# Performance work log

Measured on AMD Instinct MI355X. Metric: run time of the kernel, lower is better.

## Reference

```python
import jax, jax.numpy as jnp
import numpy as np

DIM = 2048
NUM_HEADS = 16
HEAD_DIM = DIM // NUM_HEADS  # 128
LATENT = 512
THETA = 10000.0


def rotate_half(x):
    # interleaved rotate: (x0,x1,x2,x3,...) -> (-x1,x0,-x3,x2,...)
    x1 = x[..., ::2]
    x2 = x[..., 1::2]
    return jnp.stack((-x2, x1), axis=-1).reshape(x.shape)


def apply_rope(x, sin, cos):
    return x * cos + rotate_half(x) * sin


def setup_inputs() -> dict:
    key = jax.random.key(0)
    ks = jax.random.split(key, 6)
    s_in = 1.0 / np.sqrt(DIM)
    s_lat = 1.0 / np.sqrt(LATENT)
    x = jax.random.normal(ks[0], (2, 2048, DIM), dtype=jnp.float32)
    Wq = jax.random.normal(ks[1], (DIM, DIM), dtype=jnp.float32) * s_in
    Wdkv = jax.random.normal(ks[2], (DIM, 2 * LATENT), dtype=jnp.float32) * s_in
    Wuk = jax.random.normal(ks[3], (LATENT, DIM), dtype=jnp.float32) * s_lat
    Wuv = jax.random.normal(ks[4], (LATENT, DIM), dtype=jnp.float32) * s_lat
    Wo = jax.random.normal(ks[5], (DIM, DIM), dtype=jnp.float32) * s_in
    return {"x": x, "Wq": Wq, "Wdkv": Wdkv, "Wuk": Wuk, "Wuv": Wuv, "Wo": Wo}


def reference(x, Wq, Wdkv, Wuk, Wuv, Wo):
    b, s, _ = x.shape
    # q projection -> [b, h, s, hd]
    q = (x @ Wq).reshape(b, s, NUM_HEADS, HEAD_DIM).transpose(0, 2, 1, 3)
    # low-rank latent down-projection, then up-project K and V
    dkv = x @ Wdkv  # [b, s, 2*L]
    dk, dv = dkv[..., :LATENT], dkv[..., LATENT:]
    k = (dk @ Wuk).reshape(b, s, NUM_HEADS, HEAD_DIM).transpose(0, 2, 1, 3)
    v = (dv @ Wuv).reshape(b, s, NUM_HEADS, HEAD_DIM).transpose(0, 2, 1, 3)
    # RoPE cache (concatenated freqs, matching the torch module)
    inv_freq = 1.0 / (THETA ** (jnp.arange(0, HEAD_DIM, 2, dtype=jnp.float32) / HEAD_DIM))
    t = jnp.arange(s, dtype=jnp.float32)
    freqs = t[:, None] * inv_freq[None, :]          # [s, hd/2]
    emb = jnp.concatenate([freqs, freqs], axis=-1)  # [s, hd]
    sin, cos = jnp.sin(emb), jnp.cos(emb)
    q = apply_rope(q, sin, cos)
    k = apply_rope(k, sin, cos)
    # SDPA (no mask, no dropout): scale = 1/sqrt(head_dim)
    scores = jnp.einsum('bhqd,bhkd->bhqk', q, k) / jnp.sqrt(jnp.float32(HEAD_DIM))
    attn = jax.nn.softmax(scores, axis=-1)
    out = jnp.einsum('bhqk,bhkd->bhqd', attn, v)
    out = out.transpose(0, 2, 1, 3).reshape(b, s, DIM)
    return out @ Wo
```

## Files before the change

### kernel.cpp

```cpp
#include <hip/hip_runtime.h>
#include <hip/hip_bf16.h>
#include <stdint.h>

typedef __attribute__((ext_vector_type(8))) __bf16 bf16x8;
typedef __attribute__((ext_vector_type(4))) float f32x4;

__device__ __forceinline__ unsigned short f2bf(float f) {
  union { float f; unsigned u; } v; v.f = f;
  unsigned r = v.u + 0x7FFFu + ((v.u >> 16) & 1u);
  return (unsigned short)(r >> 16);
}

__device__ __forceinline__ float fast_exp2(float x) {
#if __has_builtin(__builtin_amdgcn_exp2f)
  return __builtin_amdgcn_exp2f(x);
#else
  return exp2f(x);
#endif
}

__device__ __forceinline__ void gload_lds16(const void* g, void* l) {
  __builtin_amdgcn_global_load_lds((const __attribute__((address_space(1))) void*)g,
                                   (__attribute__((address_space(3))) void*)l,
                                   16, 0, 0);
}

__global__ __launch_bounds__(256) void k_prep(
    const float* __restrict__ x, unsigned short* __restrict__ xb,
    const float* __restrict__ Wq, unsigned short* __restrict__ WqT,
    const float* __restrict__ Wdkv, unsigned short* __restrict__ WdkvT,
    const float* __restrict__ Wuk, unsigned short* __restrict__ WukT,
    const float* __restrict__ Wuv, unsigned short* __restrict__ WuvT,
    float* __restrict__ cosT, float* __restrict__ sinT) {
  const int bid = blockIdx.x;
  const int tid = threadIdx.x;
  if (bid < 8192) {
    int i = (bid * 256 + tid) * 4;
    float4 v = *reinterpret_cast<const float4*>(x + i);
    ushort4 o;
    o.x = f2bf(v.x); o.y = f2bf(v.y); o.z = f2bf(v.z); o.w = f2bf(v.w);
    *reinterpret_cast<ushort4*>(xb + i) = o;
    return;
  }
  if (bid >= 16384) {
    int idx = (bid - 16384) * 256 + tid;
    int t = idx >> 6, j = idx & 63;
    float inv = powf(10000.f, -(float)j / 64.f);
    float ang = (float)t * inv;
    cosT[idx] = cosf(ang);
    sinT[idx] = sinf(ang);
    return;
  }
  const float* in; unsigned short* out; int K, N, lid;
  if (bid < 12288)      { in = Wq;   out = WqT;   K = 2048; N = 2048; lid = bid - 8192; }
  else if (bid < 14336) { in = Wdkv; out = WdkvT; K = 2048; N = 1024; lid = bid - 12288; }
  else if (bid < 15360) { in = Wuk;  out = WukT;  K = 512;  N = 2048; lid = bid - 14336; }
  else                  { in = Wuv;  out = WuvT;  K = 512;  N = 2048; lid = bid - 15360; }
  const int ntx = N >> 5;
  const int nt = lid % ntx, kt = lid / ntx;
  __shared__ float t[32][33];
  const int tx = tid & 31, ty = tid >> 5;
#pragma unroll
  for (int i = 0; i < 4; i++)
    t[ty + i * 8][tx] = in[(size_t)(kt * 32 + ty + i * 8) * N + nt * 32 + tx];
  __syncthreads();
#pragma unroll
  for (int i = 0; i < 4; i++)
    out[(size_t)(nt * 32 + ty + i * 8) * K + kt * 32 + tx] = f2bf(t[tx][ty + i * 8]);
}

__global__ __launch_bounds__(256) void k_transpose_cvt(const float* __restrict__ in,
                                                       unsigned short* __restrict__ out,
                                                       int K, int N) {
  __shared__ float t[32][33];
  int nt = blockIdx.x, kt = blockIdx.y;
  int tx = threadIdx.x, ty = threadIdx.y;
#pragma unroll
  for (int i = 0; i < 4; i++)
    t[ty + i * 8][tx] = in[(size_t)(kt * 32 + ty + i * 8) * N + nt * 32 + tx];
  __syncthreads();
#pragma unroll
  for (int i = 0; i < 4; i++)
    out[(size_t)(nt * 32 + ty + i * 8) * K + kt * 32 + tx] = f2bf(t[tx][ty + i * 8]);
}

template <int EPI>
__global__ __launch_bounds__(256, 2) void k_gemm(
    const unsigned short* __restrict__ A, int lda,
    const unsigned short* __restrict__ BT, int ldb,
    void* __restrict__ Cout, void* __restrict__ Cout2, int M, int N, int K,
    const float* __restrict__ cosT, const float* __restrict__ sinT) {
  __shared__ __attribute__((aligned(16))) unsigned short As[128 * 64];
  __shared__ __attribute__((aligned(16))) unsigned short Bs[128 * 64];
  const int tid = threadIdx.x;
  const int lane = tid & 63;
  const int w = tid >> 6;
  const int wr = w >> 1, wc = w & 1;
  const int m0 = blockIdx.y * 128, n0 = blockIdx.x * 128;

  f32x4 acc[4][4] = {};

  const int srow = w * 8 + (lane >> 3);
  const int sch = (lane & 7) * 8;
  const unsigned short* gA = A + (size_t)(m0 + srow) * lda + sch;
  const unsigned short* gB = BT + (size_t)(n0 + srow) * ldb + sch;
  unsigned short* lA = &As[srow * 64 + sch];
  unsigned short* lB = &Bs[srow * 64 + sch];

  for (int kt = 0; kt < K; kt += 64) {
    __syncthreads();
#pragma unroll
    for (int i = 0; i < 4; i++) {
      gload_lds16(gA + (size_t)(i * 32) * lda + kt, lA + i * 32 * 64);
      gload_lds16(gB + (size_t)(i * 32) * ldb + kt, lB + i * 32 * 64);
    }
    __syncthreads();
#pragma unroll
    for (int kk = 0; kk < 64; kk += 32) {
      bf16x8 af[4], bfr[4];
#pragma unroll
      for (int m = 0; m < 4; m++)
        af[m] = *reinterpret_cast<const bf16x8*>(&As[(wr * 64 + m * 16 + (lane & 15)) * 64 + kk + (lane >> 4) * 8]);
#pragma unroll
      for (int n = 0; n < 4; n++)
        bfr[n] = *reinterpret_cast<const bf16x8*>(&Bs[(wc * 64 + n * 16 + (lane & 15)) * 64 + kk + (lane >> 4) * 8]);
#pragma unroll
      for (int m = 0; m < 4; m++)
#pragma unroll
        for (int n = 0; n < 4; n++) {
          if (EPI == 3)
            acc[m][n] = __builtin_amdgcn_mfma_f32_16x16x32_bf16(bfr[n], af[m], acc[m][n], 0, 0, 0);
          else
            acc[m][n] = __builtin_amdgcn_mfma_f32_16x16x32_bf16(af[m], bfr[n], acc[m][n], 0, 0, 0);
        }
    }
  }

  const int rl = (lane >> 4) * 4;
  const int cl = lane & 15;
#pragma unroll
  for (int m = 0; m < 4; m++)
#pragma unroll
    for (int n = 0; n < 4; n++)
#pragma unroll
      for (int r = 0; r < 4; r++) {
        float v = acc[m][n][r];
        if (EPI == 4) {
          int gr = m0 + wr * 64 + m * 16 + rl + r;
          int gc = n0 + wc * 64 + n * 16 + cl;
          ((float*)Cout)[(size_t)gr * N + gc] = v;
        } else if (EPI == 1) {
          int gr = m0 + wr * 64 + m * 16 + rl + r;
          int gc = n0 + wc * 64 + n * 16 + cl;
          int b = gr >> 11, s = gr & 2047, h = gc >> 7, d = gc & 127;
          float p = __shfl_xor(v, 1);
          float c = cosT[s * 64 + (d & 63)];
          float sn = sinT[s * 64 + (d & 63)];
          v = v * c + ((d & 1) ? p : -p) * sn;
          ((unsigned short*)Cout)[((size_t)(b * 16 + h) * 2048 + s) * 128 + d] = f2bf(v);
        } else if (EPI == 5) {
          int gr = m0 + wr * 64 + m * 16 + rl + r;
          int gc = n0 + wc * 64 + n * 16 + cl;
          if (n0 < 2048) {
            int b = gr >> 11, s = gr & 2047, h = gc >> 7, d = gc & 127;
            float p = __shfl_xor(v, 1);
            float c = cosT[s * 64 + (d & 63)];
            float sn = sinT[s * 64 + (d & 63)];
            v = v * c + ((d & 1) ? p : -p) * sn;
            ((unsigned short*)Cout)[((size_t)(b * 16 + h) * 2048 + s) * 128 + d] = f2bf(v);
          } else {
            ((unsigned short*)Cout2)[(size_t)gr * 1024 + (gc - 2048)] = f2bf(v);
          }
        } else {
          int gd = n0 + wc * 64 + n * 16 + rl + r;
          int gs = m0 + wr * 64 + m * 16 + cl;
          int b = gs >> 11, s = gs & 2047, h = gd >> 7, d = gd & 127;
          ((unsigned short*)Cout)[((size_t)(b * 16 + h) * 128 + d) * 2048 + s] = f2bf(v);
        }
      }
}

__global__ __launch_bounds__(256, 2) void k_attn(
    const unsigned short* __restrict__ Q,
    const unsigned short* __restrict__ Kt,
    const unsigned short* __restrict__ Vt,
    unsigned short* __restrict__ O) {
  __shared__ __attribute__((aligned(16))) unsigned short Kls[2][64 * 128];
  __shared__ __attribute__((aligned(16))) unsigned short Vls[2][128 * 64];
  __shared__ __attribute__((aligned(16))) unsigned short Pls[128 * 64];
  const int flat = blockIdx.x + (blockIdx.y << 4);
  const int swz = (flat & 7) * 64 + (flat >> 3);
  const int qt = swz & 15, bh = swz >> 4;
  const int tid = threadIdx.x, lane = tid & 63, w = tid >> 6;
  const unsigned short* Qh = Q + (size_t)bh * 2048 * 128;
  const unsigned short* Kh = Kt + (size_t)bh * 2048 * 128;
  const unsigned short* Vh = Vt + (size_t)bh * 128 * 2048;
  const int q0 = qt * 128;

  bf16x8 qf[2][4];
#pragma unroll
  for (int m = 0; m < 2; m++)
#pragma unroll
    for (int kd = 0; kd < 4; kd++) {
      int row = q0 + w * 32 + m * 16 + (lane & 15);
      int k = kd * 32 + (lane >> 4) * 8;
      qf[m][kd] = *reinterpret_cast<const bf16x8*>(Qh + (size_t)row * 128 + k);
    }

  f32x4 accO[2][8] = {};
  float lsum[2] = {0.f, 0.f};

  const int kr0 = w * 4 + (lane >> 4);
  const int kcb = lane & 15;
  const int vr0 = w * 8 + (lane >> 3);
  const int vcb = lane & 7;

  auto stage = [&](int buf, int kt) {
#pragma unroll
    for (int i = 0; i < 4; i++) {
      int rr = kr0 + i * 16;
      gload_lds16(Kh + (size_t)(kt * 64 + rr) * 128 + ((kcb ^ (rr & 7)) * 8),
                  (char*)Kls + buf * 16384 + rr * 256 + kcb * 16);
    }
#pragma unroll
    for (int i = 0; i < 4; i++) {
      int rr = vr0 + i * 32;
      gload_lds16(Vh + (size_t)rr * 2048 + kt * 64 + ((vcb ^ (rr & 7)) * 8),
                  (char*)Vls + buf * 16384 + rr * 128 + vcb * 16);
    }
  };

  stage(0, 0);
  __syncthreads();

  const float CL2 = 0.08838834764831845f * 1.44269504088896f;

  for (int kt = 0; kt < 32; kt++) {
    const int cur = kt & 1;
    if (kt + 1 < 32) stage(cur ^ 1, kt + 1);

    f32x4 accT[4][2] = {};
#pragma unroll
    for (int kd = 0; kd < 4; kd++) {
      bf16x8 kf[4];
#pragma unroll
      for (int n = 0; n < 4; n++) {
        int row = n * 16 + (lane & 15);
        int byte = cur * 16384 + row * 256 + (((kd * 32 + (lane >> 4) * 8) * 2) ^ ((row & 7) << 4));
        kf[n] = *reinterpret_cast<const bf16x8*>((const char*)Kls + byte);
      }
      __builtin_amdgcn_s_setprio(1);
#pragma unroll
      for (int n = 0; n < 4; n++)
#pragma unroll
        for (int m = 0; m < 2; m++)
          accT[n][m] = __builtin_amdgcn_mfma_f32_16x16x32_bf16(kf[n], qf[m][kd], accT[n][m], 0, 0, 0);
      __builtin_amdgcn_s_setprio(0);
    }

#pragma unroll
    for (int n = 0; n < 4; n++)
#pragma unroll
      for (int m = 0; m < 2; m++) {
        float p0 = fast_exp2(accT[n][m][0] * CL2);
        float p1 = fast_exp2(accT[n][m][1] * CL2);
        float p2 = fast_exp2(accT[n][m][2] * CL2);
        float p3 = fast_exp2(accT[n][m][3] * CL2);
        lsum[m] += (p0 + p1) + (p2 + p3);
        unsigned pk0, pk1;
        asm("v_cvt_pk_bf16_f32 %0, %1, %2" : "=v"(pk0) : "v"(p0), "v"(p1));
        asm("v_cvt_pk_bf16_f32 %0, %1, %2" : "=v"(pk1) : "v"(p2), "v"(p3));
        int row = w * 32 + m * 16 + (lane & 15);
        int kcol = n * 16 + (lane >> 4) * 4;
        int byte = row * 128 + ((kcol * 2) ^ ((row & 7) << 4));
        uint2 pk = {pk0, pk1};
        *reinterpret_cast<uint2*>((char*)Pls + byte) = pk;
      }

#pragma unroll
    for (int kk = 0; kk < 2; kk++) {
      bf16x8 pf[2], vf[8];
#pragma unroll
      for (int m = 0; m < 2; m++) {
        int row = w * 32 + m * 16 + (lane & 15);
        int byte = row * 128 + (((kk * 32 + (lane >> 4) * 8) * 2) ^ ((row & 7) << 4));
        pf[m] = *reinterpret_cast<const bf16x8*>((const char*)Pls + byte);
      }
#pragma unroll
      for (int n = 0; n < 8; n++) {
        int row = n * 16 + (lane & 15);
        int byte = cur * 16384 + row * 128 + (((kk * 32 + (lane >> 4) * 8) * 2) ^ ((row & 7) << 4));
        vf[n] = *reinterpret_cast<const bf16x8*>((const char*)Vls + byte);
      }
      __builtin_amdgcn_s_setprio(1);
#pragma unroll
      for (int m = 0; m < 2; m++)
#pragma unroll
        for (int n = 0; n < 8; n++)
          accO[m][n] = __builtin_amdgcn_mfma_f32_16x16x32_bf16(pf[m], vf[n], accO[m][n], 0, 0, 0);
      __builtin_amdgcn_s_setprio(0);
    }

    __syncthreads();
  }

  const int rl = (lane >> 4) * 4;
  float rv[2][4];
#pragma unroll
  for (int m = 0; m < 2; m++) {
    float s = lsum[m];
    s += __shfl_xor(s, 16);
    s += __shfl_xor(s, 32);
    float inv = 1.0f / s;
#pragma unroll
    for (int r = 0; r < 4; r++) rv[m][r] = __shfl(inv, rl + r);
  }

  const int b = bh >> 4, h = bh & 15;
#pragma unroll
  for (int m = 0; m < 2; m++)
#pragma unroll
    for (int n = 0; n < 8; n++)
#pragma unroll
      for (int r = 0; r < 4; r++) {
        int s = q0 + w * 32 + m * 16 + rl + r;
        int d = n * 16 + (lane & 15);
        O[((size_t)(b * 2048 + s)) * 2048 + h * 128 + d] = f2bf(accO[m][n][r] * rv[m][r]);
      }
}


extern "C" void kernel_launch(void* const* d_in, const int* in_sizes, int n_in,
                              void* d_out, int out_size, void* d_ws, size_t ws_size,
                              hipStream_t stream) {
  const float* x    = (const float*)d_in[0];
  const float* Wq   = (const float*)d_in[1];
  const float* Wdkv = (const float*)d_in[2];
  const float* Wuk  = (const float*)d_in[3];
  const float* Wuv  = (const float*)d_in[4];
  const float* Wo   = (const float*)d_in[5];

  char* ws = (char*)d_ws;
  unsigned short* xb    = (unsigned short*)(ws + 0);
  unsigned short* WqT   = (unsigned short*)(ws + 16777216);
  unsigned short* WdkvT = (unsigned short*)(ws + 25165824);
  unsigned short* WukT  = (unsigned short*)(ws + 29360128);
  unsigned short* WuvT  = (unsigned short*)(ws + 31457280);
  unsigned short* dkv   = (unsigned short*)(ws + 33554432);
  unsigned short* q_att = (unsigned short*)(ws + 41943040);
  unsigned short* k_att = (unsigned short*)(ws + 58720256);
  unsigned short* vT    = (unsigned short*)(ws + 75497472);
  float* cosT           = (float*)(ws + 92274688);
  float* sinT           = (float*)(ws + 92798976);

  k_prep<<<16896, 256, 0, stream>>>(x, xb, Wq, WqT, Wdkv, WdkvT, Wuk, WukT, Wuv, WuvT, cosT, sinT);

  k_gemm<5><<<dim3(24, 32), 256, 0, stream>>>(xb, 2048, WqT, 2048, q_att, dkv, 4096, 3072, 2048, cosT, sinT);
  k_transpose_cvt<<<dim3(64, 64), dim3(32, 8), 0, stream>>>(Wo, WqT, 2048, 2048);
  k_gemm<1><<<dim3(16, 32), 256, 0, stream>>>(dkv, 1024, WukT, 512, k_att, nullptr, 4096, 2048, 512, cosT, sinT);
  k_gemm<3><<<dim3(16, 32), 256, 0, stream>>>(dkv + 512, 1024, WuvT, 512, vT, nullptr, 4096, 2048, 512, nullptr, nullptr);
  k_attn<<<dim3(16, 32), 256, 0, stream>>>(q_att, k_att, vT, xb);
  k_gemm<4><<<dim3(16, 32), 256, 0, stream>>>(xb, 2048, WqT, 2048, (float*)d_out, nullptr, 4096, 2048, 2048, nullptr, nullptr);
}
```

Measured before the change: 250.8 us.

## Fold Wo transpose into V GEMM launch and add XCD block remapping

Removes the standalone Wo transpose/convert kernel by appending extra blocks to the V up-projection GEMM grid that perform the transpose serially over many tiles. Also remaps workgroup IDs in all GEMMs so consecutive tiles are distributed across the 8 XCDs. This aims to cut a launch and improve cache locality. The risk is that the 32 transpose blocks each loop over 128 tiles and may extend the V GEMM's tail.

```diff
diff --git a/kernel.cpp b/kernel.cpp
--- a/kernel.cpp
+++ b/kernel.cpp
@@ -69,21 +69,6 @@
     out[(size_t)(nt * 32 + ty + i * 8) * K + kt * 32 + tx] = f2bf(t[tx][ty + i * 8]);
 }
 
-__global__ __launch_bounds__(256) void k_transpose_cvt(const float* __restrict__ in,
-                                                       unsigned short* __restrict__ out,
-                                                       int K, int N) {
-  __shared__ float t[32][33];
-  int nt = blockIdx.x, kt = blockIdx.y;
-  int tx = threadIdx.x, ty = threadIdx.y;
-#pragma unroll
-  for (int i = 0; i < 4; i++)
-    t[ty + i * 8][tx] = in[(size_t)(kt * 32 + ty + i * 8) * N + nt * 32 + tx];
-  __syncthreads();
-#pragma unroll
-  for (int i = 0; i < 4; i++)
-    out[(size_t)(nt * 32 + ty + i * 8) * K + kt * 32 + tx] = f2bf(t[tx][ty + i * 8]);
-}
-
 template <int EPI>
 __global__ __launch_bounds__(256, 2) void k_gemm(
     const unsigned short* __restrict__ A, int lda,
@@ -93,10 +78,38 @@
   __shared__ __attribute__((aligned(16))) unsigned short As[128 * 64];
   __shared__ __attribute__((aligned(16))) unsigned short Bs[128 * 64];
   const int tid = threadIdx.x;
+
+  if (EPI == 3 && blockIdx.y >= 32) {
+    const float* Win = cosT;
+    unsigned short* Wout = (unsigned short*)Cout2;
+    float (*t)[33] = (float(*)[33])As;
+    const int tx = tid & 31, ty = tid >> 5;
+    const int lid = (blockIdx.y - 32) * gridDim.x + blockIdx.x;
+    for (int it = 0; it < 128; ++it) {
+      int tile = lid * 128 + it;
+      int nt = tile & 63, kt2 = tile >> 6;
+#pragma unroll
+      for (int i = 0; i < 4; i++)
+        t[ty + i * 8][tx] = Win[(size_t)(kt2 * 32 + ty + i * 8) * 2048 + nt * 32 + tx];
+      __syncthreads();
+#pragma unroll
+      for (int i = 0; i < 4; i++)
+        Wout[(size_t)(nt * 32 + ty + i * 8) * 2048 + kt2 * 32 + tx] = f2bf(t[tx][ty + i * 8]);
+      __syncthreads();
+    }
+    return;
+  }
+
   const int lane = tid & 63;
   const int w = tid >> 6;
   const int wr = w >> 1, wc = w & 1;
-  const int m0 = blockIdx.y * 128, n0 = blockIdx.x * 128;
+
+  const int nby = (EPI == 3) ? 32 : gridDim.y;
+  const int nwg = gridDim.x * nby;
+  const int cpx = nwg >> 3;
+  int flat = blockIdx.y * gridDim.x + blockIdx.x;
+  flat = (flat & 7) * cpx + (flat >> 3);
+  const int m0 = (flat / gridDim.x) * 128, n0 = (flat % gridDim.x) * 128;
 
   f32x4 acc[4][4] = {};
 
@@ -356,9 +369,8 @@
   k_prep<<<16896, 256, 0, stream>>>(x, xb, Wq, WqT, Wdkv, WdkvT, Wuk, WukT, Wuv, WuvT, cosT, sinT);
 
   k_gemm<5><<<dim3(24, 32), 256, 0, stream>>>(xb, 2048, WqT, 2048, q_att, dkv, 4096, 3072, 2048, cosT, sinT);
-  k_transpose_cvt<<<dim3(64, 64), dim3(32, 8), 0, stream>>>(Wo, WqT, 2048, 2048);
   k_gemm<1><<<dim3(16, 32), 256, 0, stream>>>(dkv, 1024, WukT, 512, k_att, nullptr, 4096, 2048, 512, cosT, sinT);
-  k_gemm<3><<<dim3(16, 32), 256, 0, stream>>>(dkv + 512, 1024, WuvT, 512, vT, nullptr, 4096, 2048, 512, nullptr, nullptr);
+  k_gemm<3><<<dim3(16, 34), 256, 0, stream>>>(dkv + 512, 1024, WuvT, 512, vT, WqT, 4096, 2048, 512, Wo, nullptr);
   k_attn<<<dim3(16, 32), 256, 0, stream>>>(q_att, k_att, vT, xb);
   k_gemm<4><<<dim3(16, 32), 256, 0, stream>>>(xb, 2048, WqT, 2048, (float*)d_out, nullptr, 4096, 2048, 2048, nullptr, nullptr);
 }
```

After: 308.9 us. 1.23x slower.
